# Optimization experiments

Measured on AMD Instinct MI355X. Metric: run time of the kernel, lower is better.

The kernel has to match this reference:

```python
import jax, jax.numpy as jnp
import numpy as np
from jax import lax

B, T, QD, ED, AD = 256, 512, 1024, 512, 128
NF, KS = 32, 31  # location filters, kernel size
PAD = (KS - 1) // 2


def setup_inputs() -> dict:
    key = jax.random.key(0)
    ks = jax.random.split(key, 12)
    query = jax.random.normal(ks[0], (B, QD), jnp.float32)
    inputs = jax.random.normal(ks[1], (B, T, ED), jnp.float32)
    processed_inputs = jax.random.normal(ks[2], (B, T, AD), jnp.float32)
    mask = jnp.ones((B, T), jnp.bool_)
    # init_states()
    attention_weights = jnp.zeros((B, T), jnp.float32)
    attention_weights_cum = jnp.zeros((B, T), jnp.float32)
    alpha = jnp.concatenate([jnp.ones((B, 1)), jnp.full((B, T - 1), 1e-7)], axis=1).astype(jnp.float32)
    u = 0.5 * jnp.ones((B, 1), jnp.float32)
    # parameters (xavier-ish scale)
    Wq = jax.random.normal(ks[3], (QD, AD), jnp.float32) * 0.03
    conv_w = jax.random.normal(ks[4], (NF, 2, KS), jnp.float32) * 0.1  # OIH
    Wloc = jax.random.normal(ks[5], (NF, AD), jnp.float32) * 0.1
    v_w = jax.random.normal(ks[6], (AD, 1), jnp.float32) * 0.1
    v_b = jnp.zeros((1,), jnp.float32)
    ta_w = jax.random.normal(ks[7], (ED + QD, 1), jnp.float32) * 0.02
    ta_b = jnp.zeros((1,), jnp.float32)
    return dict(query=query, inputs=inputs, processed_inputs=processed_inputs, mask=mask,
                attention_weights=attention_weights, attention_weights_cum=attention_weights_cum,
                alpha=alpha, u=u, Wq=Wq, conv_w=conv_w, Wloc=Wloc, v_w=v_w, v_b=v_b,
                ta_w=ta_w, ta_b=ta_b)


def reference(query, inputs, processed_inputs, mask, attention_weights,
              attention_weights_cum, alpha, u, Wq, conv_w, Wloc, v_w, v_b, ta_w, ta_b):
    # location-sensitive energies
    att_cat = jnp.stack([attention_weights, attention_weights_cum], axis=1)  # [B,2,T]
    loc = lax.conv_general_dilated(att_cat, conv_w, (1,), [(PAD, PAD)],
                                   dimension_numbers=('NCH', 'OIH', 'NCH'))  # [B,NF,T]
    proc_attn = jnp.einsum('bft,fa->bta', loc, Wloc)                         # [B,T,AD]
    proc_query = (query @ Wq)[:, None, :]                                    # [B,1,AD]
    energies = (jnp.tanh(proc_query + proc_attn + processed_inputs) @ v_w + v_b)[..., 0]  # [B,T]
    energies = jnp.where(mask, energies, -jnp.inf)
    alignment = jax.nn.softmax(energies, axis=-1)
    # forward attention recursion (training mode, no forward_attn_mask)
    shifted = jnp.pad(alpha[:, :-1], ((0, 0), (1, 0)))
    alpha_new = ((1.0 - u) * alpha + u * shifted + 1e-8) * alignment
    alpha_new = alpha_new / jnp.sum(alpha_new, axis=1, keepdims=True)
    context = jnp.einsum('bt,btd->bd', alpha_new, inputs)                    # [B,ED]
    # transition agent (state update; computed for faithfulness)
    u_new = jax.nn.sigmoid(jnp.concatenate([context, query], axis=-1) @ ta_w + ta_b)
    del u_new
    return context
```

## Files before the change

### kernel.cpp

```cpp
#include <hip/hip_runtime.h>

#define BB 256
#define TT 512
#define QD 1024
#define ED 512
#define AD 128
#define NF 32
#define KS 31
#define PADL 15
#define TCHUNK 256

typedef float f32x4 __attribute__((ext_vector_type(4)));

__device__ __forceinline__ float tanh_fast(float x) {
    float ex = __expf(2.0f * x);
    return 1.0f - 2.0f / (ex + 1.0f);
}

__device__ __forceinline__ float dpp_xor1(float x) {
    int y = __builtin_amdgcn_update_dpp(0, __float_as_int(x), 0xB1, 0xF, 0xF, true);
    return x + __int_as_float(y);
}
__device__ __forceinline__ float dpp_xor2(float x) {
    int y = __builtin_amdgcn_update_dpp(0, __float_as_int(x), 0x4E, 0xF, 0xF, true);
    return x + __int_as_float(y);
}
__device__ __forceinline__ float dpp_xor4(float x) {
    int y = __builtin_amdgcn_update_dpp(0, __float_as_int(x), 0x141, 0xF, 0xF, true);
    return x + __int_as_float(y);
}
__device__ __forceinline__ float dpp_xor8(float x) {
    int y = __builtin_amdgcn_update_dpp(0, __float_as_int(x), 0x140, 0xF, 0xF, true);
    return x + __int_as_float(y);
}
__device__ __forceinline__ float wave_sum64(float x) {
    x = dpp_xor1(x);
    x = dpp_xor2(x);
    x = dpp_xor4(x);
    x = dpp_xor8(x);
    int xi = __float_as_int(x);
    float r0  = __int_as_float(__builtin_amdgcn_readlane(xi, 0));
    float r16 = __int_as_float(__builtin_amdgcn_readlane(xi, 16));
    float r32 = __int_as_float(__builtin_amdgcn_readlane(xi, 32));
    float r48 = __int_as_float(__builtin_amdgcn_readlane(xi, 48));
    return (r0 + r16) + (r32 + r48);
}

__global__ __launch_bounds__(256) void k_pq(const float* __restrict__ query,
                                            const float* __restrict__ Wq,
                                            float* __restrict__ pq) {
    int b = blockIdx.x;
    int tid = threadIdx.x;
    __shared__ float qs[QD];
    __shared__ float part[256];
    for (int i = tid; i < QD; i += 256) qs[i] = query[(size_t)b * QD + i];
    __syncthreads();
    int half = tid >> 7;
    int a = tid & 127;
    int kbase = half * 512;
    const float* wp = Wq + (size_t)kbase * AD + a;
    float acc = 0.f;
#pragma unroll 8
    for (int k = 0; k < 512; ++k)
        acc = fmaf(qs[kbase + k], wp[(size_t)k * AD], acc);
    part[tid] = acc;
    __syncthreads();
    if (tid < 128) pq[(size_t)b * AD + tid] = part[tid] + part[tid + 128];
}

__global__ __launch_bounds__(256) void k_energies(
    const float* __restrict__ attW, const float* __restrict__ attC,
    const float* __restrict__ convw, const float* __restrict__ Wloc,
    const float* __restrict__ pq, const float* __restrict__ pin,
    const float* __restrict__ vw, const float* __restrict__ vb,
    const float* __restrict__ alpha, const float* __restrict__ uArr,
    float* __restrict__ qOut) {
    int b = blockIdx.x;
    int t0 = blockIdx.y * TCHUNK;
    int tid = threadIdx.x;

    __shared__ float sA[TCHUNK + 2 * PADL];
    __shared__ float sC[TCHUNK + 2 * PADL];
    __shared__ float sAl[TCHUNK + 1];
    __shared__ float sLoc[TCHUNK * 36];

    for (int i = tid; i < TCHUNK + 2 * PADL; i += 256) {
        int t = t0 + i - PADL;
        float a = 0.f, c = 0.f;
        if (t >= 0 && t < TT) {
            a = attW[(size_t)b * TT + t];
            c = attC[(size_t)b * TT + t];
        }
        sA[i] = a;
        sC[i] = c;
    }
    for (int i = tid; i < TCHUNK + 1; i += 256) {
        int t = t0 + i - 1;
        sAl[i] = (t >= 0) ? alpha[(size_t)b * TT + t] : 0.f;
    }
    __syncthreads();

    {
        float winA[KS], winC[KS];
#pragma unroll
        for (int k = 0; k < KS; ++k) {
            winA[k] = sA[tid + k];
            winC[k] = sC[tid + k];
        }
        float* lrow = sLoc + tid * 36;
        for (int f = 0; f < NF; ++f) {
            const float* cwa = convw + f * (2 * KS);
            float acc = 0.f;
#pragma unroll
            for (int k = 0; k < KS; ++k) {
                acc = fmaf(cwa[k], winA[k], acc);
                acc = fmaf(cwa[KS + k], winC[k], acc);
            }
            lrow[f] = acc;
        }
    }
    __syncthreads();

    int wid = tid >> 6, lane = tid & 63;
    float2 w2[NF];
#pragma unroll
    for (int f = 0; f < NF; ++f)
        w2[f] = ((const float2*)(Wloc + f * AD))[lane];
    float2 pq2 = ((const float2*)(pq + (size_t)b * AD))[lane];
    float2 vw2 = ((const float2*)vw)[lane];
    float vbv = vb[0];
    float u = uArr[b];

    for (int tt = wid; tt < TCHUNK; tt += 4) {
        int t = t0 + tt;
        const float4* lr = (const float4*)(sLoc + tt * 36);
        float pa0 = 0.f, pa1 = 0.f;
#pragma unroll
        for (int j = 0; j < 8; ++j) {
            float4 Lv = lr[j];
            pa0 = fmaf(Lv.x, w2[4 * j + 0].x, pa0);
            pa1 = fmaf(Lv.x, w2[4 * j + 0].y, pa1);
            pa0 = fmaf(Lv.y, w2[4 * j + 1].x, pa0);
            pa1 = fmaf(Lv.y, w2[4 * j + 1].y, pa1);
            pa0 = fmaf(Lv.z, w2[4 * j + 2].x, pa0);
            pa1 = fmaf(Lv.z, w2[4 * j + 2].y, pa1);
            pa0 = fmaf(Lv.w, w2[4 * j + 3].x, pa0);
            pa1 = fmaf(Lv.w, w2[4 * j + 3].y, pa1);
        }
        float2 p2 = ((const float2*)pin)[(size_t)(b * TT + t) * (AD / 2) + lane];
        float x0 = pq2.x + pa0 + p2.x;
        float x1 = pq2.y + pa1 + p2.y;
        float epart = tanh_fast(x0) * vw2.x + tanh_fast(x1) * vw2.y;
        float e = wave_sum64(epart);
        if (lane == 0) {
            float w = fmaf(1.f - u, sAl[tt + 1], u * sAl[tt] + 1e-8f);
            qOut[(size_t)b * TT + t] = w * __expf(e + vbv);
        }
    }
}

__global__ __launch_bounds__(1024) void k_ctx(
    const float* __restrict__ qIn, const float* __restrict__ inputs,
    float* __restrict__ out) {
    int b = blockIdx.x;
    int tid = threadIdx.x;
    int lane = tid & 63, wid = tid >> 6;

    __shared__ float al[TT];
    __shared__ float red[16];
    __shared__ f32x4 sacc[8][128];

    size_t base = (size_t)b * TT;
    float q = 0.f;
    if (tid < TT) {
        q = qIn[base + tid];
        al[tid] = q;
    }
    float s = wave_sum64(q);
    if (lane == 0) red[wid] = s;
    __syncthreads();
    s = 0.f;
#pragma unroll
    for (int i = 0; i < 16; ++i) s += red[i];

    int g = tid >> 7;
    int c = tid & 127;
    const f32x4* in4 = (const f32x4*)inputs;
    size_t rb = ((size_t)b * TT + (size_t)g * 64) * (ED / 4) + c;
    f32x4 acc = (f32x4)(0.f);
#pragma unroll 16
    for (int j = 0; j < 64; ++j) {
        f32x4 v = in4[rb + (size_t)j * (ED / 4)];
        float w = al[g * 64 + j];
        acc.x = fmaf(w, v.x, acc.x);
        acc.y = fmaf(w, v.y, acc.y);
        acc.z = fmaf(w, v.z, acc.z);
        acc.w = fmaf(w, v.w, acc.w);
    }
    sacc[g][c] = acc;
    __syncthreads();
    if (tid < 128) {
        f32x4 t = sacc[0][tid];
#pragma unroll
        for (int i = 1; i < 8; ++i) t += sacc[i][tid];
        float inv = 1.f / s;
        t.x *= inv; t.y *= inv; t.z *= inv; t.w *= inv;
        ((f32x4*)out)[(size_t)b * (ED / 4) + tid] = t;
    }
}

extern "C" void kernel_launch(void* const* d_in, const int* in_sizes, int n_in,
                              void* d_out, int out_size, void* d_ws, size_t ws_size,
                              hipStream_t stream) {
    (void)in_sizes; (void)n_in; (void)out_size; (void)ws_size;
    const float* query = (const float*)d_in[0];
    const float* inputs = (const float*)d_in[1];
    const float* pin   = (const float*)d_in[2];
    const float* attW  = (const float*)d_in[4];
    const float* attC  = (const float*)d_in[5];
    const float* alpha = (const float*)d_in[6];
    const float* uArr  = (const float*)d_in[7];
    const float* Wq    = (const float*)d_in[8];
    const float* convw = (const float*)d_in[9];
    const float* Wloc  = (const float*)d_in[10];
    const float* vw    = (const float*)d_in[11];
    const float* vb    = (const float*)d_in[12];

    float* ws = (float*)d_ws;
    float* pq   = ws;
    float* qBuf = pq + BB * AD;

    k_pq<<<dim3(BB), dim3(256), 0, stream>>>(query, Wq, pq);
    k_energies<<<dim3(BB, TT / TCHUNK), dim3(256), 0, stream>>>(
        attW, attC, convw, Wloc, pq, pin, vw, vb, alpha, uArr, qBuf);
    k_ctx<<<dim3(BB), dim3(1024), 0, stream>>>(qBuf, inputs, (float*)d_out);
}
```

Baseline: 135.1 us.

## Split context reduction across T segments with a separate finalize kernel

Replaces the single 1024-thread-per-batch context kernel with a 2D grid of 256-thread blocks, each reducing a 64-row segment of T and writing a partial context and partial alignment sum to workspace. A small finalize kernel then adds the partials and normalises. The aim is more, smaller blocks streaming the 268MB inputs tensor, plus nontemporal loads. The cost is an extra launch and a partial-buffer round trip through global memory.

```diff
diff --git a/kernel.cpp b/kernel.cpp
--- a/kernel.cpp
+++ b/kernel.cpp
@@ -9,6 +9,8 @@
 #define KS 31
 #define PADL 15
 #define TCHUNK 256
+#define CSEG 8
+#define CROWS (TT / CSEG)
 
 typedef float f32x4 __attribute__((ext_vector_type(4)));
 
@@ -159,54 +161,62 @@
     }
 }
 
-__global__ __launch_bounds__(1024) void k_ctx(
+__global__ __launch_bounds__(256) void k_ctx_partial(
     const float* __restrict__ qIn, const float* __restrict__ inputs,
-    float* __restrict__ out) {
-    int b = blockIdx.x;
+    float* __restrict__ partial, float* __restrict__ spart) {
+    int b = blockIdx.x, seg = blockIdx.y;
     int tid = threadIdx.x;
-    int lane = tid & 63, wid = tid >> 6;
-
-    __shared__ float al[TT];
-    __shared__ float red[16];
-    __shared__ f32x4 sacc[8][128];
-
-    size_t base = (size_t)b * TT;
-    float q = 0.f;
-    if (tid < TT) {
-        q = qIn[base + tid];
-        al[tid] = q;
-    }
-    float s = wave_sum64(q);
-    if (lane == 0) red[wid] = s;
-    __syncthreads();
-    s = 0.f;
-#pragma unroll
-    for (int i = 0; i < 16; ++i) s += red[i];
-
-    int g = tid >> 7;
+    int t0 = seg * CROWS;
+
+    __shared__ float qs[CROWS];
+    __shared__ f32x4 sacc[128];
+
+    if (tid < CROWS) qs[tid] = qIn[(size_t)b * TT + t0 + tid];
+    __syncthreads();
+
+    if (tid < 64) {
+        float s = wave_sum64(qs[tid]);
+        if (tid == 0) spart[(size_t)b * CSEG + seg] = s;
+    }
+
     int c = tid & 127;
+    int r = tid >> 7;
     const f32x4* in4 = (const f32x4*)inputs;
-    size_t rb = ((size_t)b * TT + (size_t)g * 64) * (ED / 4) + c;
+    size_t rb = ((size_t)b * TT + t0 + r) * (ED / 4) + c;
     f32x4 acc = (f32x4)(0.f);
 #pragma unroll 16
-    for (int j = 0; j < 64; ++j) {
-        f32x4 v = in4[rb + (size_t)j * (ED / 4)];
-        float w = al[g * 64 + j];
+    for (int j = 0; j < CROWS / 2; ++j) {
+        f32x4 v = __builtin_nontemporal_load(&in4[rb + (size_t)(2 * j) * (ED / 4)]);
+        float w = qs[2 * j + r];
         acc.x = fmaf(w, v.x, acc.x);
         acc.y = fmaf(w, v.y, acc.y);
         acc.z = fmaf(w, v.z, acc.z);
         acc.w = fmaf(w, v.w, acc.w);
     }
-    sacc[g][c] = acc;
-    __syncthreads();
-    if (tid < 128) {
-        f32x4 t = sacc[0][tid];
-#pragma unroll
-        for (int i = 1; i < 8; ++i) t += sacc[i][tid];
-        float inv = 1.f / s;
-        t.x *= inv; t.y *= inv; t.z *= inv; t.w *= inv;
-        ((f32x4*)out)[(size_t)b * (ED / 4) + tid] = t;
-    }
+    if (r == 1) sacc[c] = acc;
+    __syncthreads();
+    if (r == 0) {
+        f32x4 t = acc + sacc[c];
+        ((f32x4*)partial)[((size_t)(b * CSEG + seg)) * (ED / 4) + c] = t;
+    }
+}
+
+__global__ __launch_bounds__(256) void k_fin(
+    const float* __restrict__ partial, const float* __restrict__ spart,
+    float* __restrict__ out) {
+    int idx = blockIdx.x * 256 + threadIdx.x;
+    int b = idx >> 7, c = idx & 127;
+    float s = 0.f;
+#pragma unroll
+    for (int g = 0; g < CSEG; ++g) s += spart[(size_t)b * CSEG + g];
+    const f32x4* p4 = (const f32x4*)partial;
+    f32x4 acc = (f32x4)(0.f);
+#pragma unroll
+    for (int g = 0; g < CSEG; ++g)
+        acc += p4[((size_t)(b * CSEG + g)) * (ED / 4) + c];
+    float inv = 1.f / s;
+    acc.x *= inv; acc.y *= inv; acc.z *= inv; acc.w *= inv;
+    ((f32x4*)out)[idx] = acc;
 }
 
 extern "C" void kernel_launch(void* const* d_in, const int* in_sizes, int n_in,
@@ -227,11 +237,16 @@
     const float* vb    = (const float*)d_in[12];
 
     float* ws = (float*)d_ws;
-    float* pq   = ws;
-    float* qBuf = pq + BB * AD;
+    float* pq      = ws;
+    float* qBuf    = pq + BB * AD;
+    float* partial = qBuf + BB * TT;
+    float* spart   = partial + BB * CSEG * ED;
 
     k_pq<<<dim3(BB), dim3(256), 0, stream>>>(query, Wq, pq);
     k_energies<<<dim3(BB, TT / TCHUNK), dim3(256), 0, stream>>>(
         attW, attC, convw, Wloc, pq, pin, vw, vb, alpha, uArr, qBuf);
-    k_ctx<<<dim3(BB), dim3(1024), 0, stream>>>(qBuf, inputs, (float*)d_out);
-}
+    k_ctx_partial<<<dim3(BB, CSEG), dim3(256), 0, stream>>>(
+        qBuf, inputs, partial, spart);
+    k_fin<<<dim3((BB * ED / 4) / 256), dim3(256), 0, stream>>>(
+        partial, spart, (float*)d_out);
+}
```

Measured after the change: 121.5 us. 1.11x faster.

## Fuse energies and context into one warp-specialized pipelined kernel per batch

Applied to the files above, without the earlier changes.

Merges the energy kernel and the context kernel into one kernel per batch row. Eight waves compute the conv, location projection and energies for 64-timestep tiles, while four other waves accumulate the weighted sum over `inputs` for the previous tile, synchronised with block barriers. This removes the intermediate buffer round trip and one kernel launch, and overlaps the compute-bound energy work with the bandwidth-bound context read. The trade-off is fewer blocks (256 blocks of 768 threads) and only four waves streaming the large `inputs` tensor, which may leave memory bandwidth underused. Conv windows are also now read straight from global memory rather than through shared memory.

```diff
diff --git a/kernel.cpp b/kernel.cpp
--- a/kernel.cpp
+++ b/kernel.cpp
@@ -8,7 +8,10 @@
 #define NF 32
 #define KS 31
 #define PADL 15
-#define TCHUNK 256
+#define TILE 64
+#define NTILE 8
+#define ENT 512
+#define NTHR 768
 
 typedef float f32x4 __attribute__((ext_vector_type(4)));
 
@@ -34,10 +37,7 @@
     return x + __int_as_float(y);
 }
 __device__ __forceinline__ float wave_sum64(float x) {
-    x = dpp_xor1(x);
-    x = dpp_xor2(x);
-    x = dpp_xor4(x);
-    x = dpp_xor8(x);
+    x = dpp_xor1(x); x = dpp_xor2(x); x = dpp_xor4(x); x = dpp_xor8(x);
     int xi = __float_as_int(x);
     float r0  = __int_as_float(__builtin_amdgcn_readlane(xi, 0));
     float r16 = __int_as_float(__builtin_amdgcn_readlane(xi, 16));
@@ -68,144 +68,138 @@
     if (tid < 128) pq[(size_t)b * AD + tid] = part[tid] + part[tid + 128];
 }
 
-__global__ __launch_bounds__(256) void k_energies(
+__global__ __launch_bounds__(NTHR, 3) void k_mega(
     const float* __restrict__ attW, const float* __restrict__ attC,
     const float* __restrict__ convw, const float* __restrict__ Wloc,
     const float* __restrict__ pq, const float* __restrict__ pin,
     const float* __restrict__ vw, const float* __restrict__ vb,
     const float* __restrict__ alpha, const float* __restrict__ uArr,
-    float* __restrict__ qOut) {
-    int b = blockIdx.x;
-    int t0 = blockIdx.y * TCHUNK;
-    int tid = threadIdx.x;
-
-    __shared__ float sA[TCHUNK + 2 * PADL];
-    __shared__ float sC[TCHUNK + 2 * PADL];
-    __shared__ float sAl[TCHUNK + 1];
-    __shared__ float sLoc[TCHUNK * 36];
-
-    for (int i = tid; i < TCHUNK + 2 * PADL; i += 256) {
-        int t = t0 + i - PADL;
-        float a = 0.f, c = 0.f;
-        if (t >= 0 && t < TT) {
-            a = attW[(size_t)b * TT + t];
-            c = attC[(size_t)b * TT + t];
-        }
-        sA[i] = a;
-        sC[i] = c;
-    }
-    for (int i = tid; i < TCHUNK + 1; i += 256) {
-        int t = t0 + i - 1;
-        sAl[i] = (t >= 0) ? alpha[(size_t)b * TT + t] : 0.f;
-    }
-    __syncthreads();
-
-    {
-        float winA[KS], winC[KS];
-#pragma unroll
-        for (int k = 0; k < KS; ++k) {
-            winA[k] = sA[tid + k];
-            winC[k] = sC[tid + k];
-        }
-        float* lrow = sLoc + tid * 36;
-        for (int f = 0; f < NF; ++f) {
-            const float* cwa = convw + f * (2 * KS);
-            float acc = 0.f;
-#pragma unroll
-            for (int k = 0; k < KS; ++k) {
-                acc = fmaf(cwa[k], winA[k], acc);
-                acc = fmaf(cwa[KS + k], winC[k], acc);
-            }
-            lrow[f] = acc;
-        }
-    }
-    __syncthreads();
-
-    int wid = tid >> 6, lane = tid & 63;
-    float2 w2[NF];
-#pragma unroll
-    for (int f = 0; f < NF; ++f)
-        w2[f] = ((const float2*)(Wloc + f * AD))[lane];
-    float2 pq2 = ((const float2*)(pq + (size_t)b * AD))[lane];
-    float2 vw2 = ((const float2*)vw)[lane];
-    float vbv = vb[0];
-    float u = uArr[b];
-
-    for (int tt = wid; tt < TCHUNK; tt += 4) {
-        int t = t0 + tt;
-        const float4* lr = (const float4*)(sLoc + tt * 36);
-        float pa0 = 0.f, pa1 = 0.f;
-#pragma unroll
-        for (int j = 0; j < 8; ++j) {
-            float4 Lv = lr[j];
-            pa0 = fmaf(Lv.x, w2[4 * j + 0].x, pa0);
-            pa1 = fmaf(Lv.x, w2[4 * j + 0].y, pa1);
-            pa0 = fmaf(Lv.y, w2[4 * j + 1].x, pa0);
-            pa1 = fmaf(Lv.y, w2[4 * j + 1].y, pa1);
-            pa0 = fmaf(Lv.z, w2[4 * j + 2].x, pa0);
-            pa1 = fmaf(Lv.z, w2[4 * j + 2].y, pa1);
-            pa0 = fmaf(Lv.w, w2[4 * j + 3].x, pa0);
-            pa1 = fmaf(Lv.w, w2[4 * j + 3].y, pa1);
-        }
-        float2 p2 = ((const float2*)pin)[(size_t)(b * TT + t) * (AD / 2) + lane];
-        float x0 = pq2.x + pa0 + p2.x;
-        float x1 = pq2.y + pa1 + p2.y;
-        float epart = tanh_fast(x0) * vw2.x + tanh_fast(x1) * vw2.y;
-        float e = wave_sum64(epart);
-        if (lane == 0) {
-            float w = fmaf(1.f - u, sAl[tt + 1], u * sAl[tt] + 1e-8f);
-            qOut[(size_t)b * TT + t] = w * __expf(e + vbv);
-        }
-    }
-}
-
-__global__ __launch_bounds__(1024) void k_ctx(
-    const float* __restrict__ qIn, const float* __restrict__ inputs,
-    float* __restrict__ out) {
+    const float* __restrict__ inputs, float* __restrict__ out) {
     int b = blockIdx.x;
     int tid = threadIdx.x;
-    int lane = tid & 63, wid = tid >> 6;
-
-    __shared__ float al[TT];
-    __shared__ float red[16];
-    __shared__ f32x4 sacc[8][128];
-
-    size_t base = (size_t)b * TT;
-    float q = 0.f;
-    if (tid < TT) {
-        q = qIn[base + tid];
-        al[tid] = q;
-    }
-    float s = wave_sum64(q);
-    if (lane == 0) red[wid] = s;
-    __syncthreads();
-    s = 0.f;
-#pragma unroll
-    for (int i = 0; i < 16; ++i) s += red[i];
-
-    int g = tid >> 7;
-    int c = tid & 127;
+    int wid = tid >> 6, lane = tid & 63;
+    bool isEn = (tid < ENT);
+
+    __shared__ float sLoc[TILE * 36];
+    __shared__ float qsAll[TT];
+    __shared__ f32x4 sacc[128];
+    __shared__ float sS;
+
+    float2 w2[NF];
+    float2 pq2 = {0.f, 0.f}, vw2 = {0.f, 0.f};
+    float vbv = 0.f, u = 0.f;
+    if (isEn) {
+#pragma unroll
+        for (int f = 0; f < NF; ++f)
+            w2[f] = ((const float2*)(Wloc + f * AD))[lane];
+        pq2 = ((const float2*)(pq + (size_t)b * AD))[lane];
+        vw2 = ((const float2*)vw)[lane];
+        vbv = vb[0];
+        u = uArr[b];
+    }
+    int cu = tid - ENT;
+    int cc = cu & 127, cr = cu >> 7;
+    f32x4 acc = (f32x4)(0.f);
     const f32x4* in4 = (const f32x4*)inputs;
-    size_t rb = ((size_t)b * TT + (size_t)g * 64) * (ED / 4) + c;
-    f32x4 acc = (f32x4)(0.f);
-#pragma unroll 16
-    for (int j = 0; j < 64; ++j) {
-        f32x4 v = in4[rb + (size_t)j * (ED / 4)];
-        float w = al[g * 64 + j];
-        acc.x = fmaf(w, v.x, acc.x);
-        acc.y = fmaf(w, v.y, acc.y);
-        acc.z = fmaf(w, v.z, acc.z);
-        acc.w = fmaf(w, v.w, acc.w);
-    }
-    sacc[g][c] = acc;
-    __syncthreads();
-    if (tid < 128) {
-        f32x4 t = sacc[0][tid];
-#pragma unroll
-        for (int i = 1; i < 8; ++i) t += sacc[i][tid];
-        float inv = 1.f / s;
-        t.x *= inv; t.y *= inv; t.z *= inv; t.w *= inv;
-        ((f32x4*)out)[(size_t)b * (ED / 4) + tid] = t;
+
+    auto en_tile = [&](int kt) {
+        int t0 = kt * TILE;
+        int ttw = (wid << 3) + (lane >> 3);
+        int fq = lane & 7;
+        int t = t0 + ttw;
+        float winA[KS], winC[KS];
+#pragma unroll
+        for (int k = 0; k < KS; ++k) {
+            int tg = t - PADL + k;
+            bool in = (tg >= 0) && (tg < TT);
+            winA[k] = in ? attW[(size_t)b * TT + tg] : 0.f;
+            winC[k] = in ? attC[(size_t)b * TT + tg] : 0.f;
+        }
+        float* lrow = sLoc + ttw * 36 + fq * 4;
+#pragma unroll
+        for (int ff = 0; ff < 4; ++ff) {
+            const float* cwa = convw + (fq * 4 + ff) * (2 * KS);
+            float a2 = 0.f;
+#pragma unroll
+            for (int k = 0; k < KS; ++k) {
+                a2 = fmaf(cwa[k], winA[k], a2);
+                a2 = fmaf(cwa[KS + k], winC[k], a2);
+            }
+            lrow[ff] = a2;
+        }
+        for (int i = 0; i < 8; ++i) {
+            int tt = (wid << 3) + i;
+            int tg = t0 + tt;
+            const float4* lr = (const float4*)(sLoc + tt * 36);
+            float pa0 = 0.f, pa1 = 0.f;
+#pragma unroll
+            for (int j = 0; j < 8; ++j) {
+                float4 Lv = lr[j];
+                pa0 = fmaf(Lv.x, w2[4 * j + 0].x, pa0);
+                pa1 = fmaf(Lv.x, w2[4 * j + 0].y, pa1);
+                pa0 = fmaf(Lv.y, w2[4 * j + 1].x, pa0);
+                pa1 = fmaf(Lv.y, w2[4 * j + 1].y, pa1);
+                pa0 = fmaf(Lv.z, w2[4 * j + 2].x, pa0);
+                pa1 = fmaf(Lv.z, w2[4 * j + 2].y, pa1);
+                pa0 = fmaf(Lv.w, w2[4 * j + 3].x, pa0);
+                pa1 = fmaf(Lv.w, w2[4 * j + 3].y, pa1);
+            }
+            float2 p2 = ((const float2*)pin)[((size_t)b * TT + tg) * (AD / 2) + lane];
+            float x0 = pq2.x + pa0 + p2.x;
+            float x1 = pq2.y + pa1 + p2.y;
+            float epart = tanh_fast(x0) * vw2.x + tanh_fast(x1) * vw2.y;
+            float e = wave_sum64(epart);
+            if (lane == 0) {
+                float aC = alpha[(size_t)b * TT + tg];
+                float aP = (tg > 0) ? alpha[(size_t)b * TT + tg - 1] : 0.f;
+                float wq = fmaf(1.f - u, aC, u * aP + 1e-8f);
+                qsAll[tg] = wq * __expf(e + vbv);
+            }
+        }
+    };
+
+    auto ctx_tile = [&](int kt) {
+        int t0 = kt * TILE;
+        size_t rb = ((size_t)b * TT + t0 + cr) * (ED / 4) + cc;
+#pragma unroll 8
+        for (int j = 0; j < TILE / 2; ++j) {
+            f32x4 v = __builtin_nontemporal_load(&in4[rb + (size_t)(2 * j) * (ED / 4)]);
+            float w = qsAll[t0 + 2 * j + cr];
+            acc.x = fmaf(w, v.x, acc.x);
+            acc.y = fmaf(w, v.y, acc.y);
+            acc.z = fmaf(w, v.z, acc.z);
+            acc.w = fmaf(w, v.w, acc.w);
+        }
+    };
+
+    if (isEn) en_tile(0);
+    __syncthreads();
+    for (int kt = 0; kt < NTILE; ++kt) {
+        if (isEn) {
+            if (kt + 1 < NTILE) en_tile(kt + 1);
+        } else {
+            ctx_tile(kt);
+        }
+        __syncthreads();
+    }
+
+    if (tid < 64) {
+        float sv = 0.f;
+#pragma unroll
+        for (int i = 0; i < 8; ++i) sv += qsAll[tid * 8 + i];
+        sv = wave_sum64(sv);
+        if (tid == 0) sS = sv;
+    }
+    if (!isEn && cr == 1) sacc[cc] = acc;
+    __syncthreads();
+    if (!isEn && cr == 0) {
+        float inv = 1.f / sS;
+        f32x4 tot;
+        tot.x = (acc.x + sacc[cc].x) * inv;
+        tot.y = (acc.y + sacc[cc].y) * inv;
+        tot.z = (acc.z + sacc[cc].z) * inv;
+        tot.w = (acc.w + sacc[cc].w) * inv;
+        ((f32x4*)out)[(size_t)b * (ED / 4) + cc] = tot;
     }
 }
 
@@ -226,12 +220,10 @@
     const float* vw    = (const float*)d_in[11];
     const float* vb    = (const float*)d_in[12];
 
-    float* ws = (float*)d_ws;
-    float* pq   = ws;
-    float* qBuf = pq + BB * AD;
+    float* pq = (float*)d_ws;
 
     k_pq<<<dim3(BB), dim3(256), 0, stream>>>(query, Wq, pq);
-    k_energies<<<dim3(BB, TT / TCHUNK), dim3(256), 0, stream>>>(
-        attW, attC, convw, Wloc, pq, pin, vw, vb, alpha, uArr, qBuf);
-    k_ctx<<<dim3(BB), dim3(1024), 0, stream>>>(qBuf, inputs, (float*)d_out);
-}
+    k_mega<<<dim3(BB), dim3(NTHR), 0, stream>>>(
+        attW, attC, convw, Wloc, pq, pin, vw, vb, alpha, uArr, inputs,
+        (float*)d_out);
+}
```

New measurement: 416.3 us. +208.1%, slower.
